# Performance work log

Hardware: AMD Instinct MI355X
Metric: run time of the kernel (lower is better)

## Reference

```python
import jax, jax.numpy as jnp
import numpy as np

SEQ_LEN, BZ, D_IN = 512, 64, 1024
HIDDEN, D_OUT, NUM_LANG = 256, 1024, 16


def setup_inputs() -> dict:
    key = jax.random.key(0)
    ks = jax.random.split(key, 6)
    x = jax.random.normal(ks[0], (SEQ_LEN, BZ, D_IN), dtype=jnp.float32)
    lang_ids = jax.random.randint(ks[1], (BZ,), 0, NUM_LANG, dtype=jnp.int64)
    # Per-language 2-layer MLP params, stacked over the language axis.
    # Stored as [in, out] so y = x @ W + b (same math as torch Linear's x @ W.T + b).
    s1 = 1.0 / np.sqrt(D_IN)
    s2 = 1.0 / np.sqrt(HIDDEN)
    W1 = jax.random.uniform(ks[2], (NUM_LANG, D_IN, HIDDEN), jnp.float32, -s1, s1)
    b1 = jax.random.uniform(ks[3], (NUM_LANG, HIDDEN), jnp.float32, -s1, s1)
    W2 = jax.random.uniform(ks[4], (NUM_LANG, HIDDEN, D_OUT), jnp.float32, -s2, s2)
    b2 = jax.random.uniform(ks[5], (NUM_LANG, D_OUT), jnp.float32, -s2, s2)
    return {"x": x, "lang_ids": lang_ids, "W1": W1, "b1": b1, "W2": W2, "b2": b2}


def reference(x, lang_ids, W1, b1, W2, b2):
    # Gather each batch element's expert weights, then do batched GEMMs.
    # Equivalent to the torch loop (dispatch -> per-expert MLP -> combine),
    # without redundant gather/scatter passes.
    W1g = W1[lang_ids]            # [bz, d_in, hidden]
    b1g = b1[lang_ids]            # [bz, hidden]
    W2g = W2[lang_ids]            # [bz, hidden, d_out]
    b2g = b2[lang_ids]            # [bz, d_out]
    h = jnp.einsum('sbd,bdh->sbh', x, W1g) + b1g[None, :, :]
    h = jax.nn.relu(h)
    y = jnp.einsum('sbh,bho->sbo', h, W2g) + b2g[None, :, :]
    return y
```

## Files before the change

kernel.cpp:

```cpp
#include <hip/hip_runtime.h>

#define SEQ 512
#define BZ  64
#define DIN 1024
#define HID 256
#define DOUT 1024
#define NLANG 16

typedef __attribute__((ext_vector_type(8))) __bf16 bf16x8;
typedef __attribute__((ext_vector_type(4))) float f32x4;

__device__ __forceinline__ unsigned short f2bf(float f) {
    return __builtin_bit_cast(unsigned short, (__bf16)f);
}
__device__ __forceinline__ unsigned int f2bf_pack(float lo, float hi) {
    return (unsigned int)f2bf(lo) | ((unsigned int)f2bf(hi) << 16);
}
__device__ __forceinline__ void gload_lds16(const unsigned short* g, unsigned short* l) {
    __builtin_amdgcn_global_load_lds(
        (const __attribute__((address_space(1))) unsigned int*)g,
        (__attribute__((address_space(3))) unsigned int*)l, 16, 0, 0);
}

template<int K, int N>
__global__ __launch_bounds__(256)
void prep_frags(const float* __restrict__ src, unsigned short* __restrict__ dst) {
    constexpr int K32 = K / 32, N16 = N / 16;
    const int gid = blockIdx.x * 256 + threadIdx.x;
    const int l   = gid & 63;
    const int f   = gid >> 6;
    const int k32 = f & (K32 - 1);
    const int n16 = (f / K32) & (N16 - 1);
    const int lid = f / (K32 * N16);
    const float* s = src + ((long)lid * K + k32 * 32 + (l >> 4) * 8) * N + n16 * 16 + (l & 15);
    unsigned short o[8];
#pragma unroll
    for (int j = 0; j < 8; ++j) o[j] = f2bf(s[(long)j * N]);
    uint4 v;
    v.x = (unsigned int)o[0] | ((unsigned int)o[1] << 16);
    v.y = (unsigned int)o[2] | ((unsigned int)o[3] << 16);
    v.z = (unsigned int)o[4] | ((unsigned int)o[5] << 16);
    v.w = (unsigned int)o[6] | ((unsigned int)o[7] << 16);
    *(uint4*)(dst + (long)gid * 8) = v;
}

__global__ __launch_bounds__(512, 2)
void mlp_l1(const float* __restrict__ x,
            const unsigned short* __restrict__ W1f,
            const float* __restrict__ b1,
            const int* __restrict__ lang,
            unsigned short* __restrict__ h_ws) {
    __shared__ unsigned short sA[2][64 * 64];
    __shared__ unsigned short sH[64 * 256];
    char* cH = (char*)sH;

    const int b  = blockIdx.x;
    const int st = blockIdx.y;
    const int t  = threadIdx.x;
    const int l  = t & 63;
    const int w  = t >> 6;
    const int lid  = lang[b];
    const int koff = (b + st) & 15;
    const long xstride = (long)BZ * DIN;
    const float* xb = x + (long)(st * 64) * xstride + (long)b * DIN;

    const f32x4 z4 = {0.f, 0.f, 0.f, 0.f};

    f32x4 acc1[4][2];
#pragma unroll
    for (int mi = 0; mi < 4; ++mi)
#pragma unroll
        for (int ni = 0; ni < 2; ++ni) acc1[mi][ni] = z4;

    float4 xr[2];
#define LOADX(KT)                                                                  \
    {                                                                              \
        _Pragma("unroll")                                                          \
        for (int j = 0; j < 2; ++j) {                                              \
            int u = t + 512 * j, m = u >> 4, c4 = u & 15;                          \
            xr[j] = *(const float4*)(xb + (long)m * xstride + (KT) * 64 + c4 * 4); \
        }                                                                          \
    }
#define WRITEX(BUF)                                                               \
    {                                                                             \
        char* cA = (char*)sA[BUF];                                                \
        _Pragma("unroll")                                                         \
        for (int j = 0; j < 2; ++j) {                                             \
            int u = t + 512 * j, m = u >> 4, c4 = u & 15;                         \
            uint2 p;                                                              \
            p.x = f2bf_pack(xr[j].x, xr[j].y);                                    \
            p.y = f2bf_pack(xr[j].z, xr[j].w);                                    \
            *(uint2*)(cA + (((m * 128) + c4 * 8) ^ ((m & 7) << 4))) = p;          \
        }                                                                         \
    }

    const unsigned short* w1p = W1f + (((long)lid * 16 + w * 2) * 32) * 512 + (long)l * 8;

    float bvv[2];
#pragma unroll
    for (int ni = 0; ni < 2; ++ni)
        bvv[ni] = b1[lid * HID + w * 32 + ni * 16 + (l & 15)];

    LOADX(koff);
    WRITEX(0);
    bf16x8 bvp[2][2];
#pragma unroll
    for (int ni = 0; ni < 2; ++ni)
        bvp[0][ni] = __builtin_bit_cast(bf16x8,
            *(const uint4*)(w1p + (long)ni * 16384 + ((koff * 2) & 31) * 512));
    __syncthreads();

    for (int i = 0; i < 16; ++i) {
        if (i < 15) LOADX((i + 1 + koff) & 15);
        char* cA = (char*)sA[i & 1];
#pragma unroll
        for (int ks = 0; ks < 2; ++ks) {
            const int p = i * 2 + ks;
            if (p < 31) {
                const int k32n = (p + 1 + koff * 2) & 31;
#pragma unroll
                for (int ni = 0; ni < 2; ++ni)
                    bvp[(p + 1) & 1][ni] = __builtin_bit_cast(bf16x8,
                        *(const uint4*)(w1p + (long)ni * 16384 + k32n * 512));
            }
            bf16x8 av[4];
#pragma unroll
            for (int mi = 0; mi < 4; ++mi) {
                int row = mi * 16 + (l & 15);
                int ch  = ks * 4 + (l >> 4);
                av[mi] = __builtin_bit_cast(bf16x8,
                    *(const uint4*)(cA + row * 128 + ((ch ^ (row & 7)) << 4)));
            }
#pragma unroll
            for (int mi = 0; mi < 4; ++mi)
#pragma unroll
                for (int ni = 0; ni < 2; ++ni)
                    acc1[mi][ni] = __builtin_amdgcn_mfma_f32_16x16x32_bf16(
                        av[mi], bvp[p & 1][ni], acc1[mi][ni], 0, 0, 0);
        }
        if (i < 15) WRITEX((i & 1) ^ 1);
        __syncthreads();
    }

#pragma unroll
    for (int mi = 0; mi < 4; ++mi)
#pragma unroll
        for (int r = 0; r < 4; ++r) {
            int row = mi * 16 + (l >> 4) * 4 + r;
#pragma unroll
            for (int ni = 0; ni < 2; ++ni) {
                int col = w * 32 + ni * 16 + (l & 15);
                float v = acc1[mi][ni][r] + bvv[ni];
                v = v > 0.f ? v : 0.f;
                *(unsigned short*)(cH + row * 512 + (((col >> 3) ^ (row & 7)) << 4)
                                   + (col & 7) * 2) = f2bf(v);
            }
        }
    __syncthreads();

    uint4* hw = (uint4*)(h_ws + ((long)(b * 8 + st)) * 16384);
    const uint4* sq = (const uint4*)sH;
#pragma unroll
    for (int j = 0; j < 4; ++j)
        hw[t + 512 * j] = sq[t + 512 * j];
#undef LOADX
#undef WRITEX
}

__global__ __launch_bounds__(512, 2)
void mlp_l2(const unsigned short* __restrict__ h_ws,
            const unsigned short* __restrict__ W2f,
            const float* __restrict__ b2,
            const int* __restrict__ lang,
            float* __restrict__ y) {
    __shared__ unsigned short sH[64 * 256];
    char* cH = (char*)sH;

    const int b  = blockIdx.x;
    const int st = blockIdx.y;
    const int t  = threadIdx.x;
    const int l  = t & 63;
    const int w  = t >> 6;
    const int lid = lang[b];
    const int s0  = st * 64;

    const unsigned short* hw = h_ws + ((long)(b * 8 + st)) * 16384;
#pragma unroll
    for (int j = 0; j < 4; ++j) {
        int seg = w * 4 + j;
        gload_lds16(hw + seg * 512 + l * 8, sH + seg * 512);
    }

    const unsigned short* w2p = W2f + (((long)lid * 64 + w * 8) * 8) * 512 + (long)l * 8;

    const f32x4 z4 = {0.f, 0.f, 0.f, 0.f};
    bf16x8 pv[2][4];
#pragma unroll
    for (int ni = 0; ni < 4; ++ni)
        pv[0][ni] = __builtin_bit_cast(bf16x8, *(const uint4*)(w2p + (long)ni * 4096));

    __syncthreads();

    f32x4 acc[4][4];
    float b2v[4];
#pragma unroll
    for (int s = 0; s < 16; ++s) {
        const int nc = s >> 3, ks = s & 7, cur = s & 1;
        if (ks == 0) {
#pragma unroll
            for (int mi = 0; mi < 4; ++mi)
#pragma unroll
                for (int ni = 0; ni < 4; ++ni) acc[mi][ni] = z4;
#pragma unroll
            for (int ni = 0; ni < 4; ++ni)
                b2v[ni] = b2[lid * DOUT + w * 128 + nc * 64 + ni * 16 + (l & 15)];
        }
        if (s < 15) {
            const int ns = s + 1, nq = (ns >> 3) * 4, ks1 = ns & 7;
#pragma unroll
            for (int ni = 0; ni < 4; ++ni)
                pv[cur ^ 1][ni] = __builtin_bit_cast(bf16x8,
                    *(const uint4*)(w2p + (long)(nq + ni) * 4096 + ks1 * 512));
        }
        bf16x8 av2[4];
#pragma unroll
        for (int mi = 0; mi < 4; ++mi) {
            int row = mi * 16 + (l & 15);
            int ch  = ks * 4 + (l >> 4);
            av2[mi] = __builtin_bit_cast(bf16x8,
                *(const uint4*)(cH + row * 512 + ((ch ^ (row & 7)) << 4)));
        }
#pragma unroll
        for (int mi = 0; mi < 4; ++mi)
#pragma unroll
            for (int ni = 0; ni < 4; ++ni)
                acc[mi][ni] = __builtin_amdgcn_mfma_f32_16x16x32_bf16(
                    av2[mi], pv[cur][ni], acc[mi][ni], 0, 0, 0);
        if (ks == 7) {
#pragma unroll
            for (int mi = 0; mi < 4; ++mi)
#pragma unroll
                for (int r = 0; r < 4; ++r) {
                    int row = mi * 16 + (l >> 4) * 4 + r;
#pragma unroll
                    for (int ni = 0; ni < 4; ++ni) {
                        int col = w * 128 + nc * 64 + ni * 16 + (l & 15);
                        y[((long)(s0 + row) * BZ + b) * DOUT + col] =
                            acc[mi][ni][r] + b2v[ni];
                    }
                }
        }
    }
}

extern "C" void kernel_launch(void* const* d_in, const int* in_sizes, int n_in,
                              void* d_out, int out_size, void* d_ws, size_t ws_size,
                              hipStream_t stream) {
    const float* x    = (const float*)d_in[0];
    const int*   lang = (const int*)d_in[1];
    const float* W1   = (const float*)d_in[2];
    const float* b1   = (const float*)d_in[3];
    const float* W2   = (const float*)d_in[4];
    const float* b2   = (const float*)d_in[5];
    float* y = (float*)d_out;

    unsigned short* W1f = (unsigned short*)d_ws;
    unsigned short* W2f = (unsigned short*)((char*)d_ws + (size_t)NLANG * HID * DIN * 2);
    unsigned short* hws = (unsigned short*)((char*)d_ws + (size_t)NLANG * HID * DIN * 2
                                                       + (size_t)NLANG * DOUT * HID * 2);

    prep_frags<DIN, HID><<<2048, 256, 0, stream>>>(W1, W1f);
    prep_frags<HID, DOUT><<<2048, 256, 0, stream>>>(W2, W2f);

    mlp_l1<<<dim3(BZ, SEQ / 64), 512, 0, stream>>>(x, W1f, b1, lang, hws);
    mlp_l2<<<dim3(BZ, SEQ / 64), 512, 0, stream>>>(hws, W2f, b2, lang, y);
}
```

Measured before the change: 104.7 us.

## Stage fp32 x tiles via direct global-to-LDS loads and convert at fragment read

Layer-1 now stages raw fp32 x tiles into LDS with global_load_lds, using an XOR-swizzled column layout, instead of loading into registers, converting to bf16 and writing LDS. The conversion to bf16 moves to the fragment read path, just before the MFMA. It also drops the per-block k-offset rotation that staggered the start of the K loop. This frees registers and removes the VGPR round trip for x, but doubles LDS footprint and LDS read traffic and adds conversion ALU work inside the MFMA loop.

New measurement: 107.6 us. 2.8% more time.

```diff
diff --git a/kernel.cpp b/kernel.cpp
--- a/kernel.cpp
+++ b/kernel.cpp
@@ -16,7 +16,7 @@
 __device__ __forceinline__ unsigned int f2bf_pack(float lo, float hi) {
     return (unsigned int)f2bf(lo) | ((unsigned int)f2bf(hi) << 16);
 }
-__device__ __forceinline__ void gload_lds16(const unsigned short* g, unsigned short* l) {
+__device__ __forceinline__ void gload_lds16(const void* g, void* l) {
     __builtin_amdgcn_global_load_lds(
         (const __attribute__((address_space(1))) unsigned int*)g,
         (__attribute__((address_space(3))) unsigned int*)l, 16, 0, 0);
@@ -50,7 +50,7 @@
             const float* __restrict__ b1,
             const int* __restrict__ lang,
             unsigned short* __restrict__ h_ws) {
-    __shared__ unsigned short sA[2][64 * 64];
+    __shared__ float sX[2][64 * 64];
     __shared__ unsigned short sH[64 * 256];
     char* cH = (char*)sH;
 
@@ -59,40 +59,31 @@
     const int t  = threadIdx.x;
     const int l  = t & 63;
     const int w  = t >> 6;
-    const int lid  = lang[b];
-    const int koff = (b + st) & 15;
+    const int lid = lang[b];
     const long xstride = (long)BZ * DIN;
     const float* xb = x + (long)(st * 64) * xstride + (long)b * DIN;
 
+    const float* gsrc[2];
+#pragma unroll
+    for (int j = 0; j < 2; ++j) {
+        int r = (w * 2 + j) * 4 + (l >> 4);
+        int c = (l & 15) ^ (r & 15);
+        gsrc[j] = xb + (long)r * xstride + c * 4;
+    }
+#define STAGE(KT, BUF)                                                            \
+    {                                                                             \
+        _Pragma("unroll")                                                         \
+        for (int j = 0; j < 2; ++j)                                               \
+            gload_lds16(gsrc[j] + (KT) * 64,                                      \
+                        (char*)sX[BUF] + (w * 2 + j) * 1024);                     \
+    }
+
     const f32x4 z4 = {0.f, 0.f, 0.f, 0.f};
-
     f32x4 acc1[4][2];
 #pragma unroll
     for (int mi = 0; mi < 4; ++mi)
 #pragma unroll
         for (int ni = 0; ni < 2; ++ni) acc1[mi][ni] = z4;
-
-    float4 xr[2];
-#define LOADX(KT)                                                                  \
-    {                                                                              \
-        _Pragma("unroll")                                                          \
-        for (int j = 0; j < 2; ++j) {                                              \
-            int u = t + 512 * j, m = u >> 4, c4 = u & 15;                          \
-            xr[j] = *(const float4*)(xb + (long)m * xstride + (KT) * 64 + c4 * 4); \
-        }                                                                          \
-    }
-#define WRITEX(BUF)                                                               \
-    {                                                                             \
-        char* cA = (char*)sA[BUF];                                                \
-        _Pragma("unroll")                                                         \
-        for (int j = 0; j < 2; ++j) {                                             \
-            int u = t + 512 * j, m = u >> 4, c4 = u & 15;                         \
-            uint2 p;                                                              \
-            p.x = f2bf_pack(xr[j].x, xr[j].y);                                    \
-            p.y = f2bf_pack(xr[j].z, xr[j].w);                                    \
-            *(uint2*)(cA + (((m * 128) + c4 * 8) ^ ((m & 7) << 4))) = p;          \
-        }                                                                         \
-    }
 
     const unsigned short* w1p = W1f + (((long)lid * 16 + w * 2) * 32) * 512 + (long)l * 8;
 
@@ -101,35 +92,39 @@
     for (int ni = 0; ni < 2; ++ni)
         bvv[ni] = b1[lid * HID + w * 32 + ni * 16 + (l & 15)];
 
-    LOADX(koff);
-    WRITEX(0);
+    STAGE(0, 0);
     bf16x8 bvp[2][2];
 #pragma unroll
     for (int ni = 0; ni < 2; ++ni)
-        bvp[0][ni] = __builtin_bit_cast(bf16x8,
-            *(const uint4*)(w1p + (long)ni * 16384 + ((koff * 2) & 31) * 512));
+        bvp[0][ni] = __builtin_bit_cast(bf16x8, *(const uint4*)(w1p + (long)ni * 16384));
     __syncthreads();
 
-    for (int i = 0; i < 16; ++i) {
-        if (i < 15) LOADX((i + 1 + koff) & 15);
-        char* cA = (char*)sA[i & 1];
+    for (int kt = 0; kt < 16; ++kt) {
+        if (kt < 15) STAGE(kt + 1, (kt + 1) & 1);
+        const char* cX = (const char*)sX[kt & 1];
 #pragma unroll
         for (int ks = 0; ks < 2; ++ks) {
-            const int p = i * 2 + ks;
+            const int p = kt * 2 + ks;
             if (p < 31) {
-                const int k32n = (p + 1 + koff * 2) & 31;
 #pragma unroll
                 for (int ni = 0; ni < 2; ++ni)
                     bvp[(p + 1) & 1][ni] = __builtin_bit_cast(bf16x8,
-                        *(const uint4*)(w1p + (long)ni * 16384 + k32n * 512));
+                        *(const uint4*)(w1p + (long)ni * 16384 + (p + 1) * 512));
             }
             bf16x8 av[4];
 #pragma unroll
             for (int mi = 0; mi < 4; ++mi) {
-                int row = mi * 16 + (l & 15);
-                int ch  = ks * 4 + (l >> 4);
-                av[mi] = __builtin_bit_cast(bf16x8,
-                    *(const uint4*)(cA + row * 128 + ((ch ^ (row & 7)) << 4)));
+                const int r  = mi * 16 + (l & 15);
+                const int c0 = ks * 8 + (l >> 4) * 2;
+                const char* base = cX + r * 256;
+                const float4 v0 = *(const float4*)(base + ((c0 ^ (r & 15)) << 4));
+                const float4 v1 = *(const float4*)(base + (((c0 + 1) ^ (r & 15)) << 4));
+                uint4 pk;
+                pk.x = f2bf_pack(v0.x, v0.y);
+                pk.y = f2bf_pack(v0.z, v0.w);
+                pk.z = f2bf_pack(v1.x, v1.y);
+                pk.w = f2bf_pack(v1.z, v1.w);
+                av[mi] = __builtin_bit_cast(bf16x8, pk);
             }
 #pragma unroll
             for (int mi = 0; mi < 4; ++mi)
@@ -138,7 +133,6 @@
                     acc1[mi][ni] = __builtin_amdgcn_mfma_f32_16x16x32_bf16(
                         av[mi], bvp[p & 1][ni], acc1[mi][ni], 0, 0, 0);
         }
-        if (i < 15) WRITEX((i & 1) ^ 1);
         __syncthreads();
     }
 
@@ -163,8 +157,7 @@
 #pragma unroll
     for (int j = 0; j < 4; ++j)
         hw[t + 512 * j] = sq[t + 512 * j];
-#undef LOADX
-#undef WRITEX
+#undef STAGE
 }
 
 __global__ __launch_bounds__(512, 2)
```
